# Kernel optimization log

Measured on AMD Instinct MI355X. Metric: run time of the kernel, lower is better.

Reference implementation:

```python
import jax, jax.numpy as jnp
import numpy as np


def setup_inputs() -> dict:
    key = jax.random.key(0)
    k0, k1, k2, k3, k4 = jax.random.split(key, 5)
    B, C, H, W = 32, 64, 128, 128
    return {
        "x": jax.random.normal(k0, (B, C, H, W), jnp.float32),
        "w1d": jax.random.normal(k1, (64,), jnp.float32) * 0.1,   # Conv1d(1,1,k=64,s=64) weight
        "b1d": jax.random.normal(k2, (1,), jnp.float32) * 0.1,    # Conv1d bias
        "wdw": jax.random.normal(k3, (C, 1, 9, 9), jnp.float32) * 0.05,  # depthwise Conv2d weight (OIHW, groups=C)
        "bdw": jax.random.normal(k4, (C,), jnp.float32) * 0.05,   # depthwise Conv2d bias
    }


def _cov_linear(x, w1d, b1d):
    # Batched torch.cov over channels, followed by Conv1d(1,1,k=64,stride=64)
    B, C, H, W = x.shape
    f = x.reshape(B, C, H * W)
    f = f - f.mean(axis=-1, keepdims=True)
    cov = jnp.einsum('bcn,bdn->bcd', f, f) / (H * W - 1)  # [B, C, C]
    # Conv1d with kernel=stride=64 on the flattened C*C vector == segmented dot
    seg = cov.reshape(B, (C * C) // 64, 64)               # [B, C, 64] since C == 64
    return seg @ w1d + b1d                                # [B, C]


def reference(x, w1d, b1d, wdw, bdw):
    C = x.shape[1]
    c = _cov_linear(x, w1d, b1d)
    # 9x9 depthwise conv, padding=4 (same spatial size)
    y = jax.lax.conv_general_dilated(
        x, wdw, window_strides=(1, 1), padding=[(4, 4), (4, 4)],
        dimension_numbers=('NCHW', 'OIHW', 'NCHW'), feature_group_count=C)
    y = y + bdw[None, :, None, None]
    c_ = _cov_linear(y, w1d, b1d)
    raise_ch = jax.nn.softmax(c_ - c, axis=1)             # softmax over channel scores
    att = jax.nn.sigmoid(c_ * (1.0 + raise_ch))           # [B, C]
    return y * att[:, :, None, None]
```

## Files before the change

kernel.cpp:

```cpp
#include <hip/hip_runtime.h>

#define NSP 16384
#define CCH 64
#define BATCH 32
#define SPLIT 4
#define CPB (CCH / SPLIT)

#define LW 76
#define LH 40
#define LDSF (LW * LH)
#define NQ (LDSF / 4)
#define NISS 3

__device__ __forceinline__ void gload_lds16(const float* g, float* l) {
    __builtin_amdgcn_global_load_lds(
        (const __attribute__((address_space(1))) void*)g,
        (__attribute__((address_space(3))) void*)l,
        16, 0, 0);
}

__device__ __forceinline__ unsigned short f2bf(float f) {
    unsigned u = __float_as_uint(f);
    u += 0x7fffu + ((u >> 16) & 1u);
    return (unsigned short)(u >> 16);
}
__device__ __forceinline__ float bflo(unsigned u) { return __uint_as_float(u << 16); }
__device__ __forceinline__ float bfhi(unsigned u) { return __uint_as_float(u & 0xffff0000u); }

template<int YBF>
__global__ __launch_bounds__(256, 4) void conv_kernel(
    const float* __restrict__ x, const float* __restrict__ wdw,
    const float* __restrict__ bdw, const float* __restrict__ w1d,
    const float* __restrict__ zpad,
    float* __restrict__ yf, unsigned short* __restrict__ yb,
    float* __restrict__ tx_parts, float* __restrict__ ty_parts,
    float* __restrict__ S_x, float* __restrict__ S_y)
{
    const int tile = blockIdx.x;
    const int b    = blockIdx.y;
    const int sp   = blockIdx.z;
    const int tile_cx = (tile & 1) * 64;
    const int tile_ry = (tile >> 1) * 32;
    const int tid = threadIdx.x;
    const int tx = tid & 15, ty = tid >> 4;
    const int c0 = tx * 4, r0 = ty * 2;
    const int cbase = sp * CPB;

    __shared__ float bufs[2][LDSF];

    int soff[NISS]; unsigned okm = 0;
    #pragma unroll
    for (int r = 0; r < NISS; ++r) {
        int q = tid + 256 * r;
        int lrow = q / 19, lc4 = q - lrow * 19;
        int gr = tile_ry - 4 + lrow;
        int gc = tile_cx - 4 + lc4 * 4;
        soff[r] = gr * 128 + gc;
        if (q < NQ && (unsigned)gr < 128u && (unsigned)gc <= 124u) okm |= 1u << r;
    }

    const float* xb = x + (size_t)b * CCH * NSP;

#define STAGE(cc, dst) do {                                               \
        const float* plane_ = xb + (size_t)(cc) * NSP;                    \
        _Pragma("unroll")                                                 \
        for (int r_ = 0; r_ < NISS; ++r_) {                               \
            int q_ = tid + 256 * r_;                                      \
            if (q_ < NQ) {                                                \
                const float* g_ = ((okm >> r_) & 1u) ? plane_ + soff[r_]  \
                                                     : zpad;              \
                gload_lds16(g_, &(dst)[4 * q_]);                          \
            }                                                             \
        }                                                                 \
    } while (0)

    STAGE(cbase, bufs[0]);

    float txa[2][4] = {};
    float tya[2][4] = {};
    __syncthreads();

    for (int k = 0; k < CPB; ++k) {
        const int c = cbase + k;
        if (k + 1 < CPB) STAGE(c + 1, bufs[(k + 1) & 1]);

        const float* cb = bufs[k & 1];
        const float* wc = wdw + c * 81;
        float acc[2][4] = {};
        float cx[2][4];
        const float* basep = cb + r0 * LW + c0;
        #pragma unroll
        for (int ir = 0; ir < 10; ++ir) {
            const float* row = basep + ir * LW;
            float4 A  = *(const float4*)(row);
            float4 Bv = *(const float4*)(row + 4);
            float4 Cv = *(const float4*)(row + 8);
            float v[12] = {A.x, A.y, A.z, A.w, Bv.x, Bv.y, Bv.z, Bv.w,
                           Cv.x, Cv.y, Cv.z, Cv.w};
            if (ir >= 4 && ir < 6) {
                #pragma unroll
                for (int q = 0; q < 4; ++q) cx[ir - 4][q] = v[q + 4];
            }
            #pragma unroll
            for (int tv = 0; tv < 9; ++tv) {
                int o = ir - tv;
                if (o >= 0 && o < 2) {
                    #pragma unroll
                    for (int kx = 0; kx < 9; ++kx) {
                        float w = wc[tv * 9 + kx];
                        #pragma unroll
                        for (int q = 0; q < 4; ++q) acc[o][q] += w * v[kx + q];
                    }
                }
            }
        }

        const float bias = bdw[c];
        const float w1c  = w1d[c];
        float sx = 0.f, sy = 0.f;
        const size_t ybase = (size_t)(b * CCH + c) * NSP + (tile_ry + r0) * 128 + tile_cx + c0;
        #pragma unroll
        for (int o = 0; o < 2; ++o) {
            float yv[4];
            #pragma unroll
            for (int q = 0; q < 4; ++q) {
                yv[q] = acc[o][q] + bias;
                sx += cx[o][q];
                sy += yv[q];
                txa[o][q] += w1c * cx[o][q];
                tya[o][q] += w1c * yv[q];
            }
            if (YBF) {
                ushort4 s;
                s.x = f2bf(yv[0]); s.y = f2bf(yv[1]); s.z = f2bf(yv[2]); s.w = f2bf(yv[3]);
                *(ushort4*)(yb + ybase + o * 128) = s;
            } else {
                *(float4*)(yf + ybase + o * 128) = make_float4(yv[0], yv[1], yv[2], yv[3]);
            }
        }

        #pragma unroll
        for (int off = 32; off > 0; off >>= 1) {
            sx += __shfl_down(sx, off);
            sy += __shfl_down(sy, off);
        }
        if ((tid & 63) == 0) {
            atomicAdd(&S_x[b * CCH + c], sx);
            atomicAdd(&S_y[b * CCH + c], sy);
        }
        __syncthreads();
    }
#undef STAGE

    const size_t tb = ((size_t)sp * BATCH + b) * NSP + (tile_ry + r0) * 128 + tile_cx + c0;
    float* txp = tx_parts + tb;
    float* typ = ty_parts + tb;
    #pragma unroll
    for (int o = 0; o < 2; ++o) {
        *(float4*)(txp + o * 128) = make_float4(txa[o][0], txa[o][1], txa[o][2], txa[o][3]);
        *(float4*)(typ + o * 128) = make_float4(tya[o][0], tya[o][1], tya[o][2], tya[o][3]);
    }
}

__global__ __launch_bounds__(256) void collapse_kernel(
    const float4* __restrict__ parts, float4* __restrict__ tcoll)
{
    const int i = blockIdx.x * 256 + threadIdx.x;
    const int tsel = i >> 17;
    const int j = i & 131071;
    const float4* p = parts + (size_t)tsel * SPLIT * 131072;
    float4 s = p[j];
    #pragma unroll
    for (int r = 1; r < SPLIT; ++r) {
        float4 a = p[j + (size_t)r * 131072];
        s.x += a.x; s.y += a.y; s.z += a.z; s.w += a.w;
    }
    tcoll[(size_t)tsel * 131072 + j] = s;
}

template<int YBF>
__global__ __launch_bounds__(256) void dot_kernel(
    const float* __restrict__ x, const float* __restrict__ yf,
    const unsigned short* __restrict__ yb,
    const float* __restrict__ t_x, const float* __restrict__ t_y,
    float* __restrict__ dot_x, float* __restrict__ dot_y)
{
    const int bc = blockIdx.x;
    const int b  = bc >> 6;
    const int tid = threadIdx.x;
    const float4* xr  = (const float4*)(x   + (size_t)bc * NSP);
    const float4* txr = (const float4*)(t_x + (size_t)b * NSP);
    const float4* tyr = (const float4*)(t_y + (size_t)b * NSP);
    float dx = 0.f, dy = 0.f;
    if (YBF) {
        const uint4* yr = (const uint4*)(yb + (size_t)bc * NSP);
        for (int i = tid; i < NSP / 8; i += 256) {
            float4 x0 = xr[2 * i], x1 = xr[2 * i + 1];
            float4 t0 = txr[2 * i], t1 = txr[2 * i + 1];
            float4 u0 = tyr[2 * i], u1 = tyr[2 * i + 1];
            uint4 yv = yr[i];
            dx += x0.x * t0.x + x0.y * t0.y + x0.z * t0.z + x0.w * t0.w
                + x1.x * t1.x + x1.y * t1.y + x1.z * t1.z + x1.w * t1.w;
            dy += bflo(yv.x) * u0.x + bfhi(yv.x) * u0.y
                + bflo(yv.y) * u0.z + bfhi(yv.y) * u0.w
                + bflo(yv.z) * u1.x + bfhi(yv.z) * u1.y
                + bflo(yv.w) * u1.z + bfhi(yv.w) * u1.w;
        }
    } else {
        const float4* yr = (const float4*)(yf + (size_t)bc * NSP);
        for (int i = tid; i < NSP / 4; i += 256) {
            float4 xv = xr[i], tv = txr[i];
            float4 yv = yr[i], uv = tyr[i];
            dx += xv.x * tv.x + xv.y * tv.y + xv.z * tv.z + xv.w * tv.w;
            dy += yv.x * uv.x + yv.y * uv.y + yv.z * uv.z + yv.w * uv.w;
        }
    }
    #pragma unroll
    for (int off = 32; off > 0; off >>= 1) {
        dx += __shfl_down(dx, off);
        dy += __shfl_down(dy, off);
    }
    __shared__ float red[8];
    const int wid = tid >> 6;
    if ((tid & 63) == 0) { red[wid * 2] = dx; red[wid * 2 + 1] = dy; }
    __syncthreads();
    if (tid == 0) {
        dot_x[bc] = red[0] + red[2] + red[4] + red[6];
        dot_y[bc] = red[1] + red[3] + red[5] + red[7];
    }
}

__global__ __launch_bounds__(64) void att_kernel(
    const float* __restrict__ S_x, const float* __restrict__ S_y,
    const float* __restrict__ dot_x, const float* __restrict__ dot_y,
    const float* __restrict__ w1d, const float* __restrict__ b1d,
    float* __restrict__ att)
{
    const int b = blockIdx.x;
    const int c = threadIdx.x;
    const float sx = S_x[b * CCH + c];
    const float sy = S_y[b * CCH + c];
    const float w  = w1d[c];
    float tsx = w * sx, tsy = w * sy;
    #pragma unroll
    for (int off = 32; off > 0; off >>= 1) {
        tsx += __shfl_xor(tsx, off);
        tsy += __shfl_xor(tsy, off);
    }
    const float inv_n  = 1.f / 16384.f;
    const float inv_n1 = 1.f / 16383.f;
    const float bb = b1d[0];
    float cxv = (dot_x[b * CCH + c] - sx * inv_n * tsx) * inv_n1 + bb;
    float cyv = (dot_y[b * CCH + c] - sy * inv_n * tsy) * inv_n1 + bb;
    float d = cyv - cxv;
    float m = d;
    #pragma unroll
    for (int off = 32; off > 0; off >>= 1) m = fmaxf(m, __shfl_xor(m, off));
    float e = __expf(d - m);
    float s = e;
    #pragma unroll
    for (int off = 32; off > 0; off >>= 1) s += __shfl_xor(s, off);
    float r = e / s;
    float a = cyv * (1.f + r);
    att[b * CCH + c] = 1.f / (1.f + __expf(-a));
}

template<int YBF>
__global__ __launch_bounds__(256) void scale_kernel(
    const unsigned short* __restrict__ yb, float* __restrict__ out,
    const float* __restrict__ att)
{
    const size_t total8 = (size_t)BATCH * CCH * NSP / 8;
    size_t i = (size_t)blockIdx.x * blockDim.x + threadIdx.x;
    const size_t stride = (size_t)gridDim.x * blockDim.x;
    if (YBF) {
        for (; i < total8; i += stride) {
            uint4 y = ((const uint4*)yb)[i];
            float a = att[(i * 8) >> 14];
            float4 o0 = make_float4(bflo(y.x) * a, bfhi(y.x) * a,
                                    bflo(y.y) * a, bfhi(y.y) * a);
            float4 o1 = make_float4(bflo(y.z) * a, bfhi(y.z) * a,
                                    bflo(y.w) * a, bfhi(y.w) * a);
            ((float4*)out)[2 * i]     = o0;
            ((float4*)out)[2 * i + 1] = o1;
        }
    } else {
        for (; i < total8; i += stride) {
            float a = att[(i * 8) >> 14];
            float4 v0 = ((const float4*)out)[2 * i];
            float4 v1 = ((const float4*)out)[2 * i + 1];
            v0.x *= a; v0.y *= a; v0.z *= a; v0.w *= a;
            v1.x *= a; v1.y *= a; v1.z *= a; v1.w *= a;
            ((float4*)out)[2 * i]     = v0;
            ((float4*)out)[2 * i + 1] = v1;
        }
    }
}

extern "C" void kernel_launch(void* const* d_in, const int* in_sizes, int n_in,
                              void* d_out, int out_size, void* d_ws, size_t ws_size,
                              hipStream_t stream) {
    const float* x   = (const float*)d_in[0];
    const float* w1d = (const float*)d_in[1];
    const float* b1d = (const float*)d_in[2];
    const float* wdw = (const float*)d_in[3];
    const float* bdw = (const float*)d_in[4];
    float* out = (float*)d_out;
    float* fw  = (float*)d_ws;

    const size_t PARTS = (size_t)SPLIT * BATCH * NSP;
    float* tx_parts = fw;
    float* ty_parts = tx_parts + PARTS;
    float* t_x      = ty_parts + PARTS;
    float* t_y      = t_x + (size_t)BATCH * NSP;
    float* S_x      = t_y + (size_t)BATCH * NSP;
    float* S_y      = S_x + 2048;
    float* dot_x    = S_y + 2048;
    float* dot_y    = dot_x + 2048;
    float* att      = dot_y + 2048;
    float* zpad     = att + 2048;
    float* fend     = zpad + 64;
    size_t fbytes   = (size_t)((char*)fend - (char*)fw);
    fbytes = (fbytes + 255) & ~(size_t)255;
    unsigned short* yb = (unsigned short*)((char*)d_ws + fbytes);
    const size_t yb_bytes = (size_t)BATCH * CCH * NSP * 2;

    const bool ybf = (ws_size >= fbytes + yb_bytes);

    hipMemsetAsync(S_x, 0, 2 * 2048 * sizeof(float), stream);
    hipMemsetAsync(zpad, 0, 64 * sizeof(float), stream);

    if (ybf) {
        conv_kernel<1><<<dim3(8, BATCH, SPLIT), 256, 0, stream>>>(
            x, wdw, bdw, w1d, zpad, out, yb, tx_parts, ty_parts, S_x, S_y);
        collapse_kernel<<<1024, 256, 0, stream>>>((const float4*)tx_parts, (float4*)t_x);
        dot_kernel<1><<<2048, 256, 0, stream>>>(x, out, yb, t_x, t_y, dot_x, dot_y);
        att_kernel<<<BATCH, 64, 0, stream>>>(S_x, S_y, dot_x, dot_y, w1d, b1d, att);
        scale_kernel<1><<<2048, 256, 0, stream>>>(yb, out, att);
    } else {
        conv_kernel<0><<<dim3(8, BATCH, SPLIT), 256, 0, stream>>>(
            x, wdw, bdw, w1d, zpad, out, yb, tx_parts, ty_parts, S_x, S_y);
        collapse_kernel<<<1024, 256, 0, stream>>>((const float4*)tx_parts, (float4*)t_x);
        dot_kernel<0><<<2048, 256, 0, stream>>>(x, out, yb, t_x, t_y, dot_x, dot_y);
        att_kernel<<<BATCH, 64, 0, stream>>>(S_x, S_y, dot_x, dot_y, w1d, b1d, att);
        scale_kernel<0><<<2048, 256, 0, stream>>>(yb, out, att);
    }
}
```

Before: 196.4 us.

## Widen conv tile to full rows with 8 outputs per thread and swizzled LDS

Each conv block now covers a full 128-wide, 32-row strip instead of a 64x32 tile, and each thread computes 8 horizontal outputs instead of 4. LDS rows are widened and stored in an XOR-swizzled 16-byte-chunk layout, meant to avoid bank conflicts on the strided float4 reads. The aim is to cut halo overhead and LDS reads per output and to allow wider stores. In exchange, LDS use roughly doubles, occupancy drops to 2 blocks per SIMD, register pressure rises, and the grid halves.

After: 180.9 us. 1.09x faster.

```diff
diff --git a/kernel.cpp b/kernel.cpp
--- a/kernel.cpp
+++ b/kernel.cpp
@@ -6,11 +6,11 @@
 #define SPLIT 4
 #define CPB (CCH / SPLIT)
 
-#define LW 76
+#define LW 160
 #define LH 40
 #define LDSF (LW * LH)
 #define NQ (LDSF / 4)
-#define NISS 3
+#define NISS 7
 
 __device__ __forceinline__ void gload_lds16(const float* g, float* l) {
     __builtin_amdgcn_global_load_lds(
@@ -19,6 +19,8 @@
         16, 0, 0);
 }
 
+__device__ __forceinline__ int swq(int q) { return q ^ ((q >> 3) & 7); }
+
 __device__ __forceinline__ unsigned short f2bf(float f) {
     unsigned u = __float_as_uint(f);
     u += 0x7fffu + ((u >> 16) & 1u);
@@ -28,7 +30,7 @@
 __device__ __forceinline__ float bfhi(unsigned u) { return __uint_as_float(u & 0xffff0000u); }
 
 template<int YBF>
-__global__ __launch_bounds__(256, 4) void conv_kernel(
+__global__ __launch_bounds__(256, 2) void conv_kernel(
     const float* __restrict__ x, const float* __restrict__ wdw,
     const float* __restrict__ bdw, const float* __restrict__ w1d,
     const float* __restrict__ zpad,
@@ -39,11 +41,10 @@
     const int tile = blockIdx.x;
     const int b    = blockIdx.y;
     const int sp   = blockIdx.z;
-    const int tile_cx = (tile & 1) * 64;
-    const int tile_ry = (tile >> 1) * 32;
+    const int tile_ry = tile * 32;
     const int tid = threadIdx.x;
     const int tx = tid & 15, ty = tid >> 4;
-    const int c0 = tx * 4, r0 = ty * 2;
+    const int c0 = tx * 8, r0 = ty * 2;
     const int cbase = sp * CPB;
 
     __shared__ float bufs[2][LDSF];
@@ -52,12 +53,17 @@
     #pragma unroll
     for (int r = 0; r < NISS; ++r) {
         int q = tid + 256 * r;
-        int lrow = q / 19, lc4 = q - lrow * 19;
+        int lrow = q / 40, qcl = q - lrow * 40;
+        int gq = swq(qcl);
         int gr = tile_ry - 4 + lrow;
-        int gc = tile_cx - 4 + lc4 * 4;
+        int gc = gq * 4 - 4;
         soff[r] = gr * 128 + gc;
-        if (q < NQ && (unsigned)gr < 128u && (unsigned)gc <= 124u) okm |= 1u << r;
-    }
+        if (q < NQ && (unsigned)gr < 128u && gq >= 1 && gq <= 32) okm |= 1u << r;
+    }
+
+    int rb[4];
+    #pragma unroll
+    for (int j = 0; j < 4; ++j) rb[j] = r0 * LW + swq(2 * tx + j) * 4;
 
     const float* xb = x + (size_t)b * CCH * NSP;
 
@@ -76,8 +82,8 @@
 
     STAGE(cbase, bufs[0]);
 
-    float txa[2][4] = {};
-    float tya[2][4] = {};
+    float txa[2][8] = {};
+    float tya[2][8] = {};
     __syncthreads();
 
     for (int k = 0; k < CPB; ++k) {
@@ -86,30 +92,33 @@
 
         const float* cb = bufs[k & 1];
         const float* wc = wdw + c * 81;
-        float acc[2][4] = {};
-        float cx[2][4];
-        const float* basep = cb + r0 * LW + c0;
+        float acc[2][8] = {};
+        float cx[2][8];
         #pragma unroll
         for (int ir = 0; ir < 10; ++ir) {
-            const float* row = basep + ir * LW;
-            float4 A  = *(const float4*)(row);
-            float4 Bv = *(const float4*)(row + 4);
-            float4 Cv = *(const float4*)(row + 8);
-            float v[12] = {A.x, A.y, A.z, A.w, Bv.x, Bv.y, Bv.z, Bv.w,
-                           Cv.x, Cv.y, Cv.z, Cv.w};
-            if (ir >= 4 && ir < 6) {
+            float4 f0 = *(const float4*)(cb + rb[0] + ir * LW);
+            float4 f1 = *(const float4*)(cb + rb[1] + ir * LW);
+            float4 f2 = *(const float4*)(cb + rb[2] + ir * LW);
+            float4 f3 = *(const float4*)(cb + rb[3] + ir * LW);
+            float v[16] = {f0.x, f0.y, f0.z, f0.w, f1.x, f1.y, f1.z, f1.w,
+                           f2.x, f2.y, f2.z, f2.w, f3.x, f3.y, f3.z, f3.w};
+            if (ir == 4) {
                 #pragma unroll
-                for (int q = 0; q < 4; ++q) cx[ir - 4][q] = v[q + 4];
+                for (int q = 0; q < 8; ++q) cx[0][q] = v[q + 4];
+            }
+            if (ir == 5) {
+                #pragma unroll
+                for (int q = 0; q < 8; ++q) cx[1][q] = v[q + 4];
             }
             #pragma unroll
-            for (int tv = 0; tv < 9; ++tv) {
-                int o = ir - tv;
-                if (o >= 0 && o < 2) {
+            for (int o = 0; o < 2; ++o) {
+                int tv = ir - o;
+                if (tv >= 0 && tv <= 8) {
                     #pragma unroll
                     for (int kx = 0; kx < 9; ++kx) {
                         float w = wc[tv * 9 + kx];
                         #pragma unroll
-                        for (int q = 0; q < 4; ++q) acc[o][q] += w * v[kx + q];
+                        for (int q = 0; q < 8; ++q) acc[o][q] += w * v[kx + q];
                     }
                 }
             }
@@ -118,12 +127,12 @@
         const float bias = bdw[c];
         const float w1c  = w1d[c];
         float sx = 0.f, sy = 0.f;
-        const size_t ybase = (size_t)(b * CCH + c) * NSP + (tile_ry + r0) * 128 + tile_cx + c0;
+        const size_t ybase = (size_t)(b * CCH + c) * NSP + (tile_ry + r0) * 128 + c0;
         #pragma unroll
         for (int o = 0; o < 2; ++o) {
-            float yv[4];
+            float yv[8];
             #pragma unroll
-            for (int q = 0; q < 4; ++q) {
+            for (int q = 0; q < 8; ++q) {
                 yv[q] = acc[o][q] + bias;
                 sx += cx[o][q];
                 sy += yv[q];
@@ -131,11 +140,17 @@
                 tya[o][q] += w1c * yv[q];
             }
             if (YBF) {
-                ushort4 s;
-                s.x = f2bf(yv[0]); s.y = f2bf(yv[1]); s.z = f2bf(yv[2]); s.w = f2bf(yv[3]);
-                *(ushort4*)(yb + ybase + o * 128) = s;
+                uint4 s;
+                s.x = (unsigned)f2bf(yv[0]) | ((unsigned)f2bf(yv[1]) << 16);
+                s.y = (unsigned)f2bf(yv[2]) | ((unsigned)f2bf(yv[3]) << 16);
+                s.z = (unsigned)f2bf(yv[4]) | ((unsigned)f2bf(yv[5]) << 16);
+                s.w = (unsigned)f2bf(yv[6]) | ((unsigned)f2bf(yv[7]) << 16);
+                *(uint4*)(yb + ybase + o * 128) = s;
             } else {
-                *(float4*)(yf + ybase + o * 128) = make_float4(yv[0], yv[1], yv[2], yv[3]);
+                *(float4*)(yf + ybase + o * 128) =
+                    make_float4(yv[0], yv[1], yv[2], yv[3]);
+                *(float4*)(yf + ybase + o * 128 + 4) =
+                    make_float4(yv[4], yv[5], yv[6], yv[7]);
             }
         }
 
@@ -152,13 +167,15 @@
     }
 #undef STAGE
 
-    const size_t tb = ((size_t)sp * BATCH + b) * NSP + (tile_ry + r0) * 128 + tile_cx + c0;
+    const size_t tb = ((size_t)sp * BATCH + b) * NSP + (tile_ry + r0) * 128 + c0;
     float* txp = tx_parts + tb;
     float* typ = ty_parts + tb;
     #pragma unroll
     for (int o = 0; o < 2; ++o) {
-        *(float4*)(txp + o * 128) = make_float4(txa[o][0], txa[o][1], txa[o][2], txa[o][3]);
-        *(float4*)(typ + o * 128) = make_float4(tya[o][0], tya[o][1], tya[o][2], tya[o][3]);
+        *(float4*)(txp + o * 128)     = make_float4(txa[o][0], txa[o][1], txa[o][2], txa[o][3]);
+        *(float4*)(txp + o * 128 + 4) = make_float4(txa[o][4], txa[o][5], txa[o][6], txa[o][7]);
+        *(float4*)(typ + o * 128)     = make_float4(tya[o][0], tya[o][1], tya[o][2], tya[o][3]);
+        *(float4*)(typ + o * 128 + 4) = make_float4(tya[o][4], tya[o][5], tya[o][6], tya[o][7]);
     }
 }
 
@@ -331,14 +348,14 @@
     hipMemsetAsync(zpad, 0, 64 * sizeof(float), stream);
 
     if (ybf) {
-        conv_kernel<1><<<dim3(8, BATCH, SPLIT), 256, 0, stream>>>(
+        conv_kernel<1><<<dim3(4, BATCH, SPLIT), 256, 0, stream>>>(
             x, wdw, bdw, w1d, zpad, out, yb, tx_parts, ty_parts, S_x, S_y);
         collapse_kernel<<<1024, 256, 0, stream>>>((const float4*)tx_parts, (float4*)t_x);
         dot_kernel<1><<<2048, 256, 0, stream>>>(x, out, yb, t_x, t_y, dot_x, dot_y);
         att_kernel<<<BATCH, 64, 0, stream>>>(S_x, S_y, dot_x, dot_y, w1d, b1d, att);
         scale_kernel<1><<<2048, 256, 0, stream>>>(yb, out, att);
     } else {
-        conv_kernel<0><<<dim3(8, BATCH, SPLIT), 256, 0, stream>>>(
+        conv_kernel<0><<<dim3(4, BATCH, SPLIT), 256, 0, stream>>>(
             x, wdw, bdw, w1d, zpad, out, yb, tx_parts, ty_parts, S_x, S_y);
         collapse_kernel<<<1024, 256, 0, stream>>>((const float4*)tx_parts, (float4*)t_x);
         dot_kernel<0><<<2048, 256, 0, stream>>>(x, out, yb, t_x, t_y, dot_x, dot_y);
```
